# Performance work log

Hardware: AMD Instinct MI355X
Metric: run time of the kernel (lower is better)

## Reference

```python
import jax, jax.numpy as jnp
import numpy as np

D_MODEL = 256
D_STATE = 256
BATCH = 32
SEQ = 4096
RMIN, RMAX = 0.9, 0.999
NEG_SLOPE = 0.01
EPS = 1e-5


def layer_norm(x, w=None, b=None):
    m = jnp.mean(x, axis=-1, keepdims=True)
    v = jnp.var(x, axis=-1, keepdims=True)
    y = (x - m) * jax.lax.rsqrt(v + EPS)
    if w is not None:
        y = y * w + b
    return y


def leaky_relu(x):
    return jnp.where(x >= 0, x, NEG_SLOPE * x)


def setup_inputs() -> dict:
    key = jax.random.key(0)
    ks = jax.random.split(key, 12)
    x = jax.random.normal(ks[0], (BATCH, SEQ, D_MODEL), dtype=jnp.float32)
    # LRU ring init: |lambda| uniform in [rmin, rmax], phase uniform in [0, 2pi]
    u1 = jax.random.uniform(ks[1], (D_STATE,), dtype=jnp.float32)
    u2 = jax.random.uniform(ks[2], (D_STATE,), dtype=jnp.float32)
    nu_log = jnp.log(-0.5 * jnp.log(u1 * (RMAX**2 - RMIN**2) + RMIN**2))
    theta_log = jnp.log(2 * jnp.pi * u2)
    lam_mod = jnp.exp(-jnp.exp(nu_log))
    gamma_log = jnp.log(jnp.sqrt(1.0 - lam_mod**2))
    B_re = jax.random.normal(ks[3], (D_STATE, D_MODEL)) / np.sqrt(2 * D_MODEL)
    B_im = jax.random.normal(ks[4], (D_STATE, D_MODEL)) / np.sqrt(2 * D_MODEL)
    C_re = jax.random.normal(ks[5], (D_STATE, D_STATE)) / np.sqrt(D_STATE)
    C_im = jax.random.normal(ks[6], (D_STATE, D_STATE)) / np.sqrt(D_STATE)
    Dm = jax.random.normal(ks[7], (D_STATE, D_MODEL)) / np.sqrt(D_MODEL)
    Wl = jax.random.normal(ks[8], (D_MODEL, D_STATE)) / np.sqrt(D_STATE)
    bl = jax.random.normal(ks[9], (D_MODEL,)) * 0.02
    Wr = jax.random.normal(ks[10], (D_MODEL, D_STATE)) / np.sqrt(D_STATE)
    br = jax.random.normal(ks[11], (D_MODEL,)) * 0.02
    ones_m = jnp.ones((D_MODEL,), jnp.float32)
    zeros_m = jnp.zeros((D_MODEL,), jnp.float32)
    ones_s = jnp.ones((D_STATE,), jnp.float32)
    zeros_s = jnp.zeros((D_STATE,), jnp.float32)
    return {
        "x": x,
        "ln1_w": ones_m, "ln1_b": zeros_m,
        "nu_log": nu_log, "theta_log": theta_log, "gamma_log": gamma_log,
        "B_re": B_re, "B_im": B_im, "C_re": C_re, "C_im": C_im, "Dm": Dm,
        "ln2_w": ones_s, "ln2_b": zeros_s,
        "Wl": Wl, "bl": bl, "Wr": Wr, "br": br,
        "ln4_w": ones_m, "ln4_b": zeros_m,
    }


def reference(x, ln1_w, ln1_b, nu_log, theta_log, gamma_log, B_re, B_im,
              C_re, C_im, Dm, ln2_w, ln2_b, Wl, bl, Wr, br, ln4_w, ln4_b):
    # pre-norm + residual skip
    x1 = layer_norm(x, ln1_w, ln1_b)          # [B, T, d_model]
    skip = x1
    u = leaky_relu(x1)
    # LRU: h_t = lambda * h_{t-1} + gamma * (B u_t); y = Re(C h) + D u
    lam_mod = jnp.exp(-jnp.exp(nu_log))
    theta = jnp.exp(theta_log)
    lr = lam_mod * jnp.cos(theta)             # [N]
    li = lam_mod * jnp.sin(theta)
    gam = jnp.exp(gamma_log)
    bu_re = gam * jnp.einsum('btd,nd->btn', u, B_re)  # [B, T, N]
    bu_im = gam * jnp.einsum('btd,nd->btn', u, B_im)
    bu_re_t = jnp.swapaxes(bu_re, 0, 1)       # [T, B, N]
    bu_im_t = jnp.swapaxes(bu_im, 0, 1)

    def step(carry, inp):
        hr, hi = carry
        br_t, bi_t = inp
        hr2 = lr * hr - li * hi + br_t
        hi2 = lr * hi + li * hr + bi_t
        return (hr2, hi2), (hr2, hi2)

    h0 = (jnp.zeros((x.shape[0], lr.shape[0]), x.dtype),
          jnp.zeros((x.shape[0], lr.shape[0]), x.dtype))
    (hr_last, hi_last), (hr, hi) = jax.lax.scan(step, h0, (bu_re_t, bu_im_t))
    hr = jnp.swapaxes(hr, 0, 1)               # [B, T, N]
    hi = jnp.swapaxes(hi, 0, 1)
    y = (jnp.einsum('btn,mn->btm', hr, C_re)
         - jnp.einsum('btn,mn->btm', hi, C_im)
         + jnp.einsum('btd,md->btm', u, Dm))  # [B, T, d_state]
    # post-norm + nonlinearity
    y = leaky_relu(layer_norm(y, ln2_w, ln2_b))
    # gated bilinear MLP
    xl = layer_norm(y @ Wl.T + bl)            # no affine
    xr = layer_norm(y @ Wr.T + br)
    out = layer_norm(xl * xr, ln4_w, ln4_b) + skip
    return out
```

## Files before the change

### kernel.cpp

```cpp
#include <hip/hip_runtime.h>
#include <cstdint>
#include <cstddef>

#define DEV __device__ __forceinline__

typedef unsigned short u16;
typedef short short8 __attribute__((ext_vector_type(8)));
typedef float floatx4 __attribute__((ext_vector_type(4)));

constexpr int BB = 32;
constexpr int TT = 4096;
constexpr int RR = BB * TT;
constexpr int CH = 64;
constexpr int LC = TT / CH;

constexpr size_t OFF_LAM  = 0;
constexpr size_t OFF_LAML = 2048;
constexpr size_t OFF_GAM  = 4096;
constexpr size_t OFF_B1   = 8192;
constexpr size_t OFF_B2   = OFF_B1 + (size_t)512 * 256 * 2;
constexpr size_t OFF_B3   = OFF_B2 + (size_t)256 * 768 * 2;
constexpr size_t OFF_BIG  = 2ull << 20;
constexpr size_t SZB      = (size_t)RR * 256 * 2;

DEV float bf2f(u16 u) {
    unsigned int i = ((unsigned int)u) << 16;
    float f;
    __builtin_memcpy(&f, &i, 4);
    return f;
}
DEV u16 f2bf(float f) {
    unsigned int i;
    __builtin_memcpy(&i, &f, 4);
    i += 0x7fffu + ((i >> 16) & 1u);
    return (u16)(i >> 16);
}

DEV void gload16(const void* g, void* l) {
    __builtin_amdgcn_global_load_lds(
        (const __attribute__((address_space(1))) unsigned int*)g,
        (__attribute__((address_space(3))) unsigned int*)l, 16, 0, 0);
}

__global__ __launch_bounds__(256)
void k_setup(const float* __restrict__ nu_log, const float* __restrict__ theta_log,
             const float* __restrict__ gamma_log,
             const float* __restrict__ B_re, const float* __restrict__ B_im,
             const float* __restrict__ C_re, const float* __restrict__ C_im,
             const float* __restrict__ Dm,
             const float* __restrict__ Wl, const float* __restrict__ Wr,
             char* __restrict__ ws)
{
    float2* lam  = (float2*)(ws + OFF_LAM);
    float2* lamL = (float2*)(ws + OFF_LAML);
    float*  gam  = (float*)(ws + OFF_GAM);
    u16* B1 = (u16*)(ws + OFF_B1);
    u16* B2 = (u16*)(ws + OFF_B2);
    u16* B3 = (u16*)(ws + OFF_B3);
    int g = blockIdx.x * 256 + threadIdx.x;
    int stride = gridDim.x * 256;
    if (g < 256) {
        float mod = expf(-expf(nu_log[g]));
        float th  = expf(theta_log[g]);
        float lr = mod * cosf(th), li = mod * sinf(th);
        lam[g] = make_float2(lr, li);
        gam[g] = expf(gamma_log[g]);
        float pr = 1.f, pi = 0.f;
        for (int i = 0; i < LC; i++) { float nr = pr*lr - pi*li; pi = pr*li + pi*lr; pr = nr; }
        lamL[g] = make_float2(pr, pi);
    }
    for (int i = g; i < 512*256; i += stride) {
        int n = i >> 8, d = i & 255;
        B1[i] = f2bf(n < 256 ? B_re[n*256 + d] : B_im[(n-256)*256 + d]);
    }
    for (int i = g; i < 256*768; i += stride) {
        int m = i / 768, k = i - m*768;
        float v = (k < 256) ? C_re[m*256 + k]
                : (k < 512) ? -C_im[m*256 + (k-256)]
                            : Dm[m*256 + (k-512)];
        B2[i] = f2bf(v);
    }
    for (int i = g; i < 512*256; i += stride) {
        int n = i >> 8, d = i & 255;
        B3[i] = f2bf(n < 256 ? Wl[n*256 + d] : Wr[(n-256)*256 + d]);
    }
}

__global__ __launch_bounds__(256)
void k_ln1(const float* __restrict__ x, const float* __restrict__ w, const float* __restrict__ b,
           u16* __restrict__ u, u16* __restrict__ skip)
{
    const int wv = threadIdx.x >> 6, lane = threadIdx.x & 63;
    const size_t row = (size_t)blockIdx.x * 4 + wv;
    float4 v = ((const float4*)(x + row * 256))[lane];
    float s = v.x + v.y + v.z + v.w;
    float q = v.x*v.x + v.y*v.y + v.z*v.z + v.w*v.w;
    #pragma unroll
    for (int o = 32; o; o >>= 1) { s += __shfl_xor(s, o); q += __shfl_xor(q, o); }
    const float m  = s * (1.f/256.f);
    const float rs = rsqrtf(q * (1.f/256.f) - m*m + 1e-5f);
    const float4 wv4 = ((const float4*)w)[lane];
    const float4 bv4 = ((const float4*)b)[lane];
    float y0 = (v.x - m) * rs * wv4.x + bv4.x;
    float y1 = (v.y - m) * rs * wv4.y + bv4.y;
    float y2 = (v.z - m) * rs * wv4.z + bv4.z;
    float y3 = (v.w - m) * rs * wv4.w + bv4.w;
    ((ushort4*)(skip + row * 256))[lane] = make_ushort4(f2bf(y0), f2bf(y1), f2bf(y2), f2bf(y3));
    float u0 = y0 >= 0.f ? y0 : 0.01f * y0;
    float u1 = y1 >= 0.f ? y1 : 0.01f * y1;
    float u2 = y2 >= 0.f ? y2 : 0.01f * y2;
    float u3 = y3 >= 0.f ? y3 : 0.01f * y3;
    ((ushort4*)(u + row * 256))[lane] = make_ushort4(f2bf(u0), f2bf(u1), f2bf(u2), f2bf(u3));
}

__global__ __launch_bounds__(256)
void k_gemm1(const u16* __restrict__ A0, const u16* __restrict__ Bmat,
             u16* __restrict__ O0, u16* __restrict__ O1, const float* __restrict__ p0)
{
    __shared__ alignas(16) u16 As[2][128 * 64];
    __shared__ alignas(16) u16 Bs[2][128 * 64];
    const int wid = threadIdx.x >> 6, lane = threadIdx.x & 63;
    const int rowbase = blockIdx.x * 128;
    const int ct = blockIdx.y;
    const u16* Bbase = Bmat + (size_t)ct * 128 * 256;
    const int srow  = lane >> 3;
    const int sslot = (lane & 7) ^ srow;
    floatx4 acc[4][4] = {};

    auto stage = [&](int kt, int pb) {
        int kofs = kt * 64;
        #pragma unroll
        for (int i = 0; i < 4; i++) {
            int grp = wid * 4 + i;
            int row = grp * 8 + srow;
            gload16(A0 + (size_t)(rowbase + row) * 256 + kofs + sslot * 8,
                    (char*)&As[pb][0] + grp * 1024);
            gload16(Bbase + (size_t)row * 256 + kofs + sslot * 8,
                    (char*)&Bs[pb][0] + grp * 1024);
        }
    };

    stage(0, 0);
    const int wm = wid >> 1, wn = wid & 1;
    for (int kt = 0; kt < 4; ++kt) {
        const int pb = kt & 1;
        if (kt + 1 < 4) {
            stage(kt + 1, pb ^ 1);
            asm volatile("s_waitcnt vmcnt(8)" ::: "memory");
        } else {
            asm volatile("s_waitcnt vmcnt(0)" ::: "memory");
        }
        __builtin_amdgcn_s_barrier();
        short8 af[2][4], bfr[2][4];
        #pragma unroll
        for (int kk = 0; kk < 2; kk++) {
            const int rslot = (kk * 4 + (lane >> 4)) ^ (lane & 7);
            #pragma unroll
            for (int mi = 0; mi < 4; mi++)
                af[kk][mi] = *(const short8*)&As[pb][(wm*64 + mi*16 + (lane & 15)) * 64 + rslot * 8];
            #pragma unroll
            for (int ni = 0; ni < 4; ni++)
                bfr[kk][ni] = *(const short8*)&Bs[pb][(wn*64 + ni*16 + (lane & 15)) * 64 + rslot * 8];
        }
        #pragma unroll
        for (int mi = 0; mi < 4; mi++)
            #pragma unroll
            for (int ni = 0; ni < 4; ni++) {
                acc[mi][ni] = __builtin_amdgcn_mfma_f32_16x16x32_bf16(af[0][mi], bfr[0][ni], acc[mi][ni], 0, 0, 0);
                acc[mi][ni] = __builtin_amdgcn_mfma_f32_16x16x32_bf16(af[1][mi], bfr[1][ni], acc[mi][ni], 0, 0, 0);
            }
        __builtin_amdgcn_s_barrier();
    }
    #pragma unroll
    for (int mi = 0; mi < 4; mi++) {
        #pragma unroll
        for (int ni = 0; ni < 4; ni++) {
            const int cc = wn*64 + ni*16 + (lane & 15);
            const int n  = ct * 128 + cc;
            u16* outp = (n < 256) ? O0 : O1;
            const int col = n & 255;
            const float scale = p0[col];
            #pragma unroll
            for (int r = 0; r < 4; r++) {
                const int row = rowbase + wm*64 + mi*16 + ((lane >> 4) << 2) + r;
                outp[(size_t)row * 256 + col] = f2bf(acc[mi][ni][r] * scale);
            }
        }
    }
}

__global__ __launch_bounds__(512)
void k_gemm2(const u16* __restrict__ Ahr, const u16* __restrict__ Ahi, const u16* __restrict__ Au,
             const u16* __restrict__ Bm, u16* __restrict__ Oy,
             const float* __restrict__ w2, const float* __restrict__ b2)
{
    __shared__ alignas(16) char smem[49152 + 4096];
    u16*   As0 = (u16*)smem;
    u16*   Bs0 = (u16*)(smem + 16384);
    float* st  = (float*)(smem + 49152);
    const int tid = threadIdx.x, wid = tid >> 6, lane = tid & 63;
    const int lanelo = lane & 15, lanehi = lane >> 4;
    const int rowbase = blockIdx.x * 128;
    const int wm = wid >> 2, wn = wid & 3;
    floatx4 acc[4][4] = {};

    auto stage = [&](int kt, int pb) {
        const u16* Asrc = (kt < 8) ? Ahr : (kt < 16) ? Ahi : Au;
        const int kofs = (kt & 7) * 32;
        { int g = tid; int row = g >> 2, slot = g & 3;
          gload16(Asrc + (size_t)(rowbase + row) * 256 + kofs + slot * 8,
                  (char*)(As0 + pb * 4096) + (wid * 64) * 16); }
        #pragma unroll
        for (int j = 0; j < 2; j++) {
            int g = j * 512 + tid; int row = g >> 2, slot = g & 3;
            gload16(Bm + (size_t)row * 768 + kt * 32 + slot * 8,
                    (char*)(Bs0 + pb * 8192) + (j * 512 + wid * 64) * 16);
        }
    };

    stage(0, 0);
    for (int kt = 0; kt < 24; ++kt) {
        const int pb = kt & 1;
        if (kt + 1 < 24) {
            stage(kt + 1, pb ^ 1);
            asm volatile("s_waitcnt vmcnt(3)" ::: "memory");
        } else {
            asm volatile("s_waitcnt vmcnt(0)" ::: "memory");
        }
        __builtin_amdgcn_s_barrier();
        short8 af[4], bfr[4];
        #pragma unroll
        for (int mi = 0; mi < 4; mi++)
            af[mi] = *(const short8*)&As0[pb*4096 + (wm*64 + mi*16 + lanelo)*32 + lanehi*8];
        #pragma unroll
        for (int ni = 0; ni < 4; ni++)
            bfr[ni] = *(const short8*)&Bs0[pb*8192 + (wn*64 + ni*16 + lanelo)*32 + lanehi*8];
        #pragma unroll
        for (int mi = 0; mi < 4; mi++)
            #pragma unroll
            for (int ni = 0; ni < 4; ni++)
                acc[mi][ni] = __builtin_amdgcn_mfma_f32_16x16x32_bf16(af[mi], bfr[ni], acc[mi][ni], 0, 0, 0);
        __builtin_amdgcn_s_barrier();
    }

    float sarr[4][4], qarr[4][4];
    #pragma unroll
    for (int mi = 0; mi < 4; mi++)
        #pragma unroll
        for (int r = 0; r < 4; r++) {
            float s = 0.f, q = 0.f;
            #pragma unroll
            for (int ni = 0; ni < 4; ni++) { float v = acc[mi][ni][r]; s += v; q += v*v; }
            sarr[mi][r] = s; qarr[mi][r] = q;
        }
    #pragma unroll
    for (int o = 1; o < 16; o <<= 1)
        #pragma unroll
        for (int mi = 0; mi < 4; mi++)
            #pragma unroll
            for (int r = 0; r < 4; r++) {
                sarr[mi][r] += __shfl_xor(sarr[mi][r], o);
                qarr[mi][r] += __shfl_xor(qarr[mi][r], o);
            }
    if (lanelo == 0) {
        #pragma unroll
        for (int mi = 0; mi < 4; mi++)
            #pragma unroll
            for (int r = 0; r < 4; r++) {
                int rw = mi*16 + lanehi*4 + r;
                st[(wid*64 + rw)*2 + 0] = sarr[mi][r];
                st[(wid*64 + rw)*2 + 1] = qarr[mi][r];
            }
    }
    __syncthreads();
    float wc[4], bc[4];
    #pragma unroll
    for (int ni = 0; ni < 4; ni++) {
        int col = wn*64 + ni*16 + lanelo;
        wc[ni] = w2[col]; bc[ni] = b2[col];
    }
    #pragma unroll
    for (int mi = 0; mi < 4; mi++)
        #pragma unroll
        for (int r = 0; r < 4; r++) {
            const int rw = mi*16 + lanehi*4 + r;
            float S = 0.f, Q = 0.f;
            #pragma unroll
            for (int ww = 0; ww < 4; ww++) {
                S += st[((wm*4 + ww)*64 + rw)*2 + 0];
                Q += st[((wm*4 + ww)*64 + rw)*2 + 1];
            }
            const float m  = S * (1.f/256.f);
            const float rs = rsqrtf(Q * (1.f/256.f) - m*m + 1e-5f);
            const size_t row = (size_t)rowbase + wm*64 + rw;
            #pragma unroll
            for (int ni = 0; ni < 4; ni++) {
                int col = wn*64 + ni*16 + lanelo;
                float v = (acc[mi][ni][r] - m) * rs * wc[ni] + bc[ni];
                v = v >= 0.f ? v : 0.01f * v;
                Oy[row * 256 + col] = f2bf(v);
            }
        }
}

__global__ __launch_bounds__(1024)
void k_gemm3f(const u16* __restrict__ Ay, const u16* __restrict__ Bm,
              const float* __restrict__ bl, const float* __restrict__ brr,
              const float* __restrict__ w4, const float* __restrict__ b4,
              const u16* __restrict__ skip, float* __restrict__ out)
{
    __shared__ alignas(16) char smem[81920];
    u16*   As0 = (u16*)smem;
    u16*   Bs0 = (u16*)(smem + 16384);
    float* st  = (float*)smem;
    float* st4 = (float*)(smem + 16384);
    const int tid = threadIdx.x, wid = tid >> 6, lane = tid & 63;
    const int lanelo = lane & 15, lanehi = lane >> 4;
    const int rowbase = blockIdx.x * 128;
    const int wm = wid >> 3, wn = wid & 7;
    floatx4 acc[4][4] = {};

    auto stage = [&](int kt, int pb) {
        const int kofs = kt * 32;
        if (tid < 512) {
            int row = tid >> 2, slot = tid & 3;
            gload16(Ay + (size_t)(rowbase + row) * 256 + kofs + slot * 8,
                    (char*)(As0 + pb * 4096) + wid * 1024);
        }
        #pragma unroll
        for (int j = 0; j < 2; j++) {
            int g = j * 1024 + tid; int row = g >> 2, slot = g & 3;
            gload16(Bm + (size_t)row * 256 + kofs + slot * 8,
                    (char*)(Bs0 + pb * 16384) + (j * 1024 + wid * 64) * 16);
        }
    };

    stage(0, 0);
    for (int kt = 0; kt < 8; ++kt) {
        const int pb = kt & 1;
        if (kt + 1 < 8) {
            stage(kt + 1, pb ^ 1);
            if (wid < 8) asm volatile("s_waitcnt vmcnt(3)" ::: "memory");
            else         asm volatile("s_waitcnt vmcnt(2)" ::: "memory");
        } else {
            asm volatile("s_waitcnt vmcnt(0)" ::: "memory");
        }
        __builtin_amdgcn_s_barrier();
        short8 af[4], bfr[4];
        #pragma unroll
        for (int mi = 0; mi < 4; mi++)
            af[mi] = *(const short8*)&As0[pb*4096 + (wm*64 + mi*16 + lanelo)*32 + lanehi*8];
        #pragma unroll
        for (int ni = 0; ni < 4; ni++) {
            const int s = wn*32 + (ni&1)*16 + (ni>>1)*256 + lanelo;
            bfr[ni] = *(const short8*)&Bs0[pb*16384 + s*32 + lanehi*8];
        }
        #pragma unroll
        for (int mi = 0; mi < 4; mi++)
            #pragma unroll
            for (int ni = 0; ni < 4; ni++)
                acc[mi][ni] = __builtin_amdgcn_mfma_f32_16x16x32_bf16(af[mi], bfr[ni], acc[mi][ni], 0, 0, 0);
        __builtin_amdgcn_s_barrier();
    }
    __syncthreads();

    float bcl[2], bcr[2];
    #pragma unroll
    for (int j = 0; j < 2; j++) {
        const int cl = wn*32 + j*16 + lanelo;
        bcl[j] = bl[cl]; bcr[j] = brr[cl];
    }
    #pragma unroll
    for (int mi = 0; mi < 4; mi++)
        #pragma unroll
        for (int r = 0; r < 4; r++) {
            acc[mi][0][r] += bcl[0]; acc[mi][1][r] += bcl[1];
            acc[mi][2][r] += bcr[0]; acc[mi][3][r] += bcr[1];
        }
    #pragma unroll
    for (int mi = 0; mi < 4; mi++)
        #pragma unroll
        for (int r = 0; r < 4; r++) {
            float a0 = acc[mi][0][r], a1 = acc[mi][1][r];
            float b0 = acc[mi][2][r], b1 = acc[mi][3][r];
            float sLv = a0 + a1, qLv = a0*a0 + a1*a1;
            float sRv = b0 + b1, qRv = b0*b0 + b1*b1;
            #pragma unroll
            for (int o = 1; o < 16; o <<= 1) {
                sLv += __shfl_xor(sLv, o); qLv += __shfl_xor(qLv, o);
                sRv += __shfl_xor(sRv, o); qRv += __shfl_xor(qRv, o);
            }
            if (lanelo == 0) {
                const int rw = mi*16 + lanehi*4 + r;
                float* p = &st[(wid*64 + rw)*4];
                p[0] = sLv; p[1] = qLv; p[2] = sRv; p[3] = qRv;
            }
        }
    __syncthreads();
    #pragma unroll
    for (int mi = 0; mi < 4; mi++)
        #pragma unroll
        for (int r = 0; r < 4; r++) {
            const int rw = mi*16 + lanehi*4 + r;
            float SL = 0.f, QL = 0.f, SR = 0.f, QR = 0.f;
            #pragma unroll
            for (int ww = 0; ww < 8; ww++) {
                const float* p = &st[((wm*8 + ww)*64 + rw)*4];
                SL += p[0]; QL += p[1]; SR += p[2]; QR += p[3];
            }
            const float mL = SL * (1.f/256.f);
            const float rsL = rsqrtf(QL * (1.f/256.f) - mL*mL + 1e-5f);
            const float mR = SR * (1.f/256.f);
            const float rsR = rsqrtf(QR * (1.f/256.f) - mR*mR + 1e-5f);
            float p0 = ((acc[mi][0][r] - mL) * rsL) * ((acc[mi][2][r] - mR) * rsR);
            float p1 = ((acc[mi][1][r] - mL) * rsL) * ((acc[mi][3][r] - mR) * rsR);
            acc[mi][0][r] = p0; acc[mi][1][r] = p1;
            float s4 = p0 + p1, q4 = p0*p0 + p1*p1;
            #pragma unroll
            for (int o = 1; o < 16; o <<= 1) {
                s4 += __shfl_xor(s4, o); q4 += __shfl_xor(q4, o);
            }
            if (lanelo == 0) {
                float* p = &st4[(wid*64 + rw)*2];
                p[0] = s4; p[1] = q4;
            }
        }
    __syncthreads();
    float w4c[2], b4c[2];
    #pragma unroll
    for (int j = 0; j < 2; j++) {
        const int col = wn*32 + j*16 + lanelo;
        w4c[j] = w4[col]; b4c[j] = b4[col];
    }
    #pragma unroll
    for (int mi = 0; mi < 4; mi++)
        #pragma unroll
        for (int r = 0; r < 4; r++) {
            const int rw = mi*16 + lanehi*4 + r;
            float S4 = 0.f, Q4 = 0.f;
            #pragma unroll
            for (int ww = 0; ww < 8; ww++) {
                const float* p = &st4[((wm*8 + ww)*64 + rw)*2];
                S4 += p[0]; Q4 += p[1];
            }
            const float m4 = S4 * (1.f/256.f);
            const float rs4 = rsqrtf(Q4 * (1.f/256.f) - m4*m4 + 1e-5f);
            const size_t row = (size_t)rowbase + wm*64 + rw;
            #pragma unroll
            for (int j = 0; j < 2; j++) {
                const int col = wn*32 + j*16 + lanelo;
                float o = (acc[mi][j][r] - m4) * rs4 * w4c[j] + b4c[j]
                        + bf2f(skip[row*256 + col]);
                out[row*256 + col] = o;
            }
        }
}

__global__ __launch_bounds__(128)
void k_scan1(const u16* __restrict__ bre, const u16* __restrict__ bim,
             float4* __restrict__ carry, const char* __restrict__ ws)
{
    const float2* lam = (const float2*)(ws + OFF_LAM);
    const int b = blockIdx.x, c = blockIdx.y, p = threadIdx.x;
    const unsigned int* pre = (const unsigned int*)bre;
    const unsigned int* pim = (const unsigned int*)bim;
    const float2 l0 = lam[2*p], l1 = lam[2*p + 1];
    float hr0 = 0, hi0 = 0, hr1 = 0, hi1 = 0;
    size_t base = ((size_t)b * TT + (size_t)c * LC) * 128 + p;
    #pragma unroll 8
    for (int j = 0; j < LC; j++) {
        unsigned int re = pre[base + (size_t)j * 128];
        unsigned int im = pim[base + (size_t)j * 128];
        float br0 = bf2f((u16)(re & 0xffff)), br1 = bf2f((u16)(re >> 16));
        float bi0 = bf2f((u16)(im & 0xffff)), bi1 = bf2f((u16)(im >> 16));
        float nr0 = fmaf(l0.x, hr0, fmaf(-l0.y, hi0, br0));
        float ni0 = fmaf(l0.x, hi0, fmaf( l0.y, hr0, bi0));
        float nr1 = fmaf(l1.x, hr1, fmaf(-l1.y, hi1, br1));
        float ni1 = fmaf(l1.x, hi1, fmaf( l1.y, hr1, bi1));
        hr0 = nr0; hi0 = ni0; hr1 = nr1; hi1 = ni1;
    }
    carry[((size_t)b * CH + c) * 128 + p] = make_float4(hr0, hi0, hr1, hi1);
}

__global__ __launch_bounds__(128)
void k_comb(float4* __restrict__ carry, const char* __restrict__ ws)
{
    const float2* lamL = (const float2*)(ws + OFF_LAML);
    const int b = blockIdx.x, p = threadIdx.x;
    const float2 L0 = lamL[2*p], L1 = lamL[2*p + 1];
    float4 prev = make_float4(0.f, 0.f, 0.f, 0.f);
    size_t base = (size_t)b * CH * 128 + p;
    float4 nxt = carry[base];
    for (int c = 0; c < CH; c++) {
        float4 cur = nxt;
        if (c + 1 < CH) nxt = carry[base + (size_t)(c + 1) * 128];
        carry[base + (size_t)c * 128] = prev;
        float nx = fmaf(L0.x, prev.x, fmaf(-L0.y, prev.y, cur.x));
        float ny = fmaf(L0.x, prev.y, fmaf( L0.y, prev.x, cur.y));
        float nz = fmaf(L1.x, prev.z, fmaf(-L1.y, prev.w, cur.z));
        float nw = fmaf(L1.x, prev.w, fmaf( L1.y, prev.z, cur.w));
        prev = make_float4(nx, ny, nz, nw);
    }
}

__global__ __launch_bounds__(128)
void k_scan2(u16* __restrict__ bre, u16* __restrict__ bim,
             const float4* __restrict__ carry, const char* __restrict__ ws)
{
    const float2* lam = (const float2*)(ws + OFF_LAM);
    const int b = blockIdx.x, c = blockIdx.y, p = threadIdx.x;
    unsigned int* pre = (unsigned int*)bre;
    unsigned int* pim = (unsigned int*)bim;
    const float2 l0 = lam[2*p], l1 = lam[2*p + 1];
    float4 h0 = carry[((size_t)b * CH + c) * 128 + p];
    float hr0 = h0.x, hi0 = h0.y, hr1 = h0.z, hi1 = h0.w;
    size_t base = ((size_t)b * TT + (size_t)c * LC) * 128 + p;
    #pragma unroll 8
    for (int j = 0; j < LC; j++) {
        size_t idx = base + (size_t)j * 128;
        unsigned int re = pre[idx];
        unsigned int im = pim[idx];
        float br0 = bf2f((u16)(re & 0xffff)), br1 = bf2f((u16)(re >> 16));
        float bi0 = bf2f((u16)(im & 0xffff)), bi1 = bf2f((u16)(im >> 16));
        float nr0 = fmaf(l0.x, hr0, fmaf(-l0.y, hi0, br0));
        float ni0 = fmaf(l0.x, hi0, fmaf( l0.y, hr0, bi0));
        float nr1 = fmaf(l1.x, hr1, fmaf(-l1.y, hi1, br1));
        float ni1 = fmaf(l1.x, hi1, fmaf( l1.y, hr1, bi1));
        hr0 = nr0; hi0 = ni0; hr1 = nr1; hi1 = ni1;
        pre[idx] = ((unsigned int)f2bf(hr1) << 16) | f2bf(hr0);
        pim[idx] = ((unsigned int)f2bf(hi1) << 16) | f2bf(hi0);
    }
}

extern "C" void kernel_launch(void* const* d_in, const int* in_sizes, int n_in,
                              void* d_out, int out_size, void* d_ws, size_t ws_size,
                              hipStream_t stream)
{
    (void)in_sizes; (void)n_in; (void)out_size; (void)ws_size;
    const float* x         = (const float*)d_in[0];
    const float* ln1_w     = (const float*)d_in[1];
    const float* ln1_b     = (const float*)d_in[2];
    const float* nu_log    = (const float*)d_in[3];
    const float* theta_log = (const float*)d_in[4];
    const float* gamma_log = (const float*)d_in[5];
    const float* B_re      = (const float*)d_in[6];
    const float* B_im      = (const float*)d_in[7];
    const float* C_re      = (const float*)d_in[8];
    const float* C_im      = (const float*)d_in[9];
    const float* Dm        = (const float*)d_in[10];
    const float* ln2_w     = (const float*)d_in[11];
    const float* ln2_b     = (const float*)d_in[12];
    const float* Wl        = (const float*)d_in[13];
    const float* bl        = (const float*)d_in[14];
    const float* Wr        = (const float*)d_in[15];
    const float* br        = (const float*)d_in[16];
    const float* ln4_w     = (const float*)d_in[17];
    const float* ln4_b     = (const float*)d_in[18];

    char* ws = (char*)d_ws;
    float* gam = (float*)(ws + OFF_GAM);
    u16* B1 = (u16*)(ws + OFF_B1);
    u16* B2 = (u16*)(ws + OFF_B2);
    u16* B3 = (u16*)(ws + OFF_B3);
    u16* u    = (u16*)(ws + OFF_BIG);
    u16* skip = (u16*)(ws + OFF_BIG + 1 * SZB);
    u16* bure = (u16*)(ws + OFF_BIG + 2 * SZB);
    u16* buim = (u16*)(ws + OFF_BIG + 3 * SZB);
    u16* y    = (u16*)(ws + OFF_BIG + 4 * SZB);
    float4* carry = (float4*)(ws + OFF_BIG + 5 * SZB);
    float* out = (float*)d_out;

    k_setup<<<dim3(256), dim3(256), 0, stream>>>(nu_log, theta_log, gamma_log,
                                                 B_re, B_im, C_re, C_im, Dm, Wl, Wr, ws);
    k_ln1<<<dim3(RR/4), dim3(256), 0, stream>>>(x, ln1_w, ln1_b, u, skip);
    k_gemm1<<<dim3(RR/128, 4), dim3(256), 0, stream>>>(u, B1, bure, buim, gam);
    k_scan1<<<dim3(BB, CH), dim3(128), 0, stream>>>(bure, buim, carry, ws);
    k_comb<<<dim3(BB), dim3(128), 0, stream>>>(carry, ws);
    k_scan2<<<dim3(BB, CH), dim3(128), 0, stream>>>(bure, buim, carry, ws);
    k_gemm2<<<dim3(RR/128), dim3(512), 0, stream>>>(bure, buim, u, B2, y, ln2_w, ln2_b);
    k_gemm3f<<<dim3(RR/128), dim3(1024), 0, stream>>>(y, B3, bl, br, ln4_w, ln4_b, skip, out);
}
```

Measured before the change: 479.6 us.

## Split fused gated-MLP GEMM into tiled GEMM plus separate layernorm epilogue kernel

Replaces the single 1024-thread fused GEMM+triple-layernorm kernel with a 256-thread swizzled, double-buffered GEMM that writes bf16 xl/xr (bias added) into the reused bure/buim buffers. A new row-wise kernel then does the two layernorms, the product, the final layernorm and the skip add. This trades extra global traffic (writing and rereading two bf16 intermediates) for a leaner GEMM with better occupancy and no cross-wave LDS reductions. It also rounds the pre-norm activations to bf16.

```diff
diff --git a/kernel.cpp b/kernel.cpp
--- a/kernel.cpp
+++ b/kernel.cpp
@@ -189,6 +189,83 @@
     }
 }
 
+__global__ __launch_bounds__(256)
+void k_gemm3(const u16* __restrict__ A0, const u16* __restrict__ Bmat,
+             u16* __restrict__ O0, u16* __restrict__ O1,
+             const float* __restrict__ p0, const float* __restrict__ p1)
+{
+    __shared__ alignas(16) u16 As[2][128 * 64];
+    __shared__ alignas(16) u16 Bs[2][128 * 64];
+    const int wid = threadIdx.x >> 6, lane = threadIdx.x & 63;
+    const int rowbase = blockIdx.x * 128;
+    const int ct = blockIdx.y;
+    const u16* Bbase = Bmat + (size_t)ct * 128 * 256;
+    const int srow  = lane >> 3;
+    const int sslot = (lane & 7) ^ srow;
+    floatx4 acc[4][4] = {};
+
+    auto stage = [&](int kt, int pb) {
+        int kofs = kt * 64;
+        #pragma unroll
+        for (int i = 0; i < 4; i++) {
+            int grp = wid * 4 + i;
+            int row = grp * 8 + srow;
+            gload16(A0 + (size_t)(rowbase + row) * 256 + kofs + sslot * 8,
+                    (char*)&As[pb][0] + grp * 1024);
+            gload16(Bbase + (size_t)row * 256 + kofs + sslot * 8,
+                    (char*)&Bs[pb][0] + grp * 1024);
+        }
+    };
+
+    stage(0, 0);
+    const int wm = wid >> 1, wn = wid & 1;
+    for (int kt = 0; kt < 4; ++kt) {
+        const int pb = kt & 1;
+        if (kt + 1 < 4) {
+            stage(kt + 1, pb ^ 1);
+            asm volatile("s_waitcnt vmcnt(8)" ::: "memory");
+        } else {
+            asm volatile("s_waitcnt vmcnt(0)" ::: "memory");
+        }
+        __builtin_amdgcn_s_barrier();
+        short8 af[2][4], bfr[2][4];
+        #pragma unroll
+        for (int kk = 0; kk < 2; kk++) {
+            const int rslot = (kk * 4 + (lane >> 4)) ^ (lane & 7);
+            #pragma unroll
+            for (int mi = 0; mi < 4; mi++)
+                af[kk][mi] = *(const short8*)&As[pb][(wm*64 + mi*16 + (lane & 15)) * 64 + rslot * 8];
+            #pragma unroll
+            for (int ni = 0; ni < 4; ni++)
+                bfr[kk][ni] = *(const short8*)&Bs[pb][(wn*64 + ni*16 + (lane & 15)) * 64 + rslot * 8];
+        }
+        #pragma unroll
+        for (int mi = 0; mi < 4; mi++)
+            #pragma unroll
+            for (int ni = 0; ni < 4; ni++) {
+                acc[mi][ni] = __builtin_amdgcn_mfma_f32_16x16x32_bf16(af[0][mi], bfr[0][ni], acc[mi][ni], 0, 0, 0);
+                acc[mi][ni] = __builtin_amdgcn_mfma_f32_16x16x32_bf16(af[1][mi], bfr[1][ni], acc[mi][ni], 0, 0, 0);
+            }
+        __builtin_amdgcn_s_barrier();
+    }
+    #pragma unroll
+    for (int mi = 0; mi < 4; mi++) {
+        #pragma unroll
+        for (int ni = 0; ni < 4; ni++) {
+            const int cc = wn*64 + ni*16 + (lane & 15);
+            const int n  = ct * 128 + cc;
+            u16* outp = (n < 256) ? O0 : O1;
+            const int col = n & 255;
+            const float badd = (n < 256 ? p0 : p1)[col];
+            #pragma unroll
+            for (int r = 0; r < 4; r++) {
+                const int row = rowbase + wm*64 + mi*16 + ((lane >> 4) << 2) + r;
+                outp[(size_t)row * 256 + col] = f2bf(acc[mi][ni][r] + badd);
+            }
+        }
+    }
+}
+
 __global__ __launch_bounds__(512)
 void k_gemm2(const u16* __restrict__ Ahr, const u16* __restrict__ Ahi, const u16* __restrict__ Au,
              const u16* __restrict__ Bm, u16* __restrict__ Oy,
@@ -303,157 +380,41 @@
         }
 }
 
-__global__ __launch_bounds__(1024)
-void k_gemm3f(const u16* __restrict__ Ay, const u16* __restrict__ Bm,
-              const float* __restrict__ bl, const float* __restrict__ brr,
-              const float* __restrict__ w4, const float* __restrict__ b4,
-              const u16* __restrict__ skip, float* __restrict__ out)
-{
-    __shared__ alignas(16) char smem[81920];
-    u16*   As0 = (u16*)smem;
-    u16*   Bs0 = (u16*)(smem + 16384);
-    float* st  = (float*)smem;
-    float* st4 = (float*)(smem + 16384);
-    const int tid = threadIdx.x, wid = tid >> 6, lane = tid & 63;
-    const int lanelo = lane & 15, lanehi = lane >> 4;
-    const int rowbase = blockIdx.x * 128;
-    const int wm = wid >> 3, wn = wid & 7;
-    floatx4 acc[4][4] = {};
-
-    auto stage = [&](int kt, int pb) {
-        const int kofs = kt * 32;
-        if (tid < 512) {
-            int row = tid >> 2, slot = tid & 3;
-            gload16(Ay + (size_t)(rowbase + row) * 256 + kofs + slot * 8,
-                    (char*)(As0 + pb * 4096) + wid * 1024);
-        }
-        #pragma unroll
-        for (int j = 0; j < 2; j++) {
-            int g = j * 1024 + tid; int row = g >> 2, slot = g & 3;
-            gload16(Bm + (size_t)row * 256 + kofs + slot * 8,
-                    (char*)(Bs0 + pb * 16384) + (j * 1024 + wid * 64) * 16);
-        }
-    };
-
-    stage(0, 0);
-    for (int kt = 0; kt < 8; ++kt) {
-        const int pb = kt & 1;
-        if (kt + 1 < 8) {
-            stage(kt + 1, pb ^ 1);
-            if (wid < 8) asm volatile("s_waitcnt vmcnt(3)" ::: "memory");
-            else         asm volatile("s_waitcnt vmcnt(2)" ::: "memory");
-        } else {
-            asm volatile("s_waitcnt vmcnt(0)" ::: "memory");
-        }
-        __builtin_amdgcn_s_barrier();
-        short8 af[4], bfr[4];
-        #pragma unroll
-        for (int mi = 0; mi < 4; mi++)
-            af[mi] = *(const short8*)&As0[pb*4096 + (wm*64 + mi*16 + lanelo)*32 + lanehi*8];
-        #pragma unroll
-        for (int ni = 0; ni < 4; ni++) {
-            const int s = wn*32 + (ni&1)*16 + (ni>>1)*256 + lanelo;
-            bfr[ni] = *(const short8*)&Bs0[pb*16384 + s*32 + lanehi*8];
-        }
-        #pragma unroll
-        for (int mi = 0; mi < 4; mi++)
-            #pragma unroll
-            for (int ni = 0; ni < 4; ni++)
-                acc[mi][ni] = __builtin_amdgcn_mfma_f32_16x16x32_bf16(af[mi], bfr[ni], acc[mi][ni], 0, 0, 0);
-        __builtin_amdgcn_s_barrier();
-    }
-    __syncthreads();
-
-    float bcl[2], bcr[2];
-    #pragma unroll
-    for (int j = 0; j < 2; j++) {
-        const int cl = wn*32 + j*16 + lanelo;
-        bcl[j] = bl[cl]; bcr[j] = brr[cl];
-    }
-    #pragma unroll
-    for (int mi = 0; mi < 4; mi++)
-        #pragma unroll
-        for (int r = 0; r < 4; r++) {
-            acc[mi][0][r] += bcl[0]; acc[mi][1][r] += bcl[1];
-            acc[mi][2][r] += bcr[0]; acc[mi][3][r] += bcr[1];
-        }
-    #pragma unroll
-    for (int mi = 0; mi < 4; mi++)
-        #pragma unroll
-        for (int r = 0; r < 4; r++) {
-            float a0 = acc[mi][0][r], a1 = acc[mi][1][r];
-            float b0 = acc[mi][2][r], b1 = acc[mi][3][r];
-            float sLv = a0 + a1, qLv = a0*a0 + a1*a1;
-            float sRv = b0 + b1, qRv = b0*b0 + b1*b1;
-            #pragma unroll
-            for (int o = 1; o < 16; o <<= 1) {
-                sLv += __shfl_xor(sLv, o); qLv += __shfl_xor(qLv, o);
-                sRv += __shfl_xor(sRv, o); qRv += __shfl_xor(qRv, o);
-            }
-            if (lanelo == 0) {
-                const int rw = mi*16 + lanehi*4 + r;
-                float* p = &st[(wid*64 + rw)*4];
-                p[0] = sLv; p[1] = qLv; p[2] = sRv; p[3] = qRv;
-            }
-        }
-    __syncthreads();
-    #pragma unroll
-    for (int mi = 0; mi < 4; mi++)
-        #pragma unroll
-        for (int r = 0; r < 4; r++) {
-            const int rw = mi*16 + lanehi*4 + r;
-            float SL = 0.f, QL = 0.f, SR = 0.f, QR = 0.f;
-            #pragma unroll
-            for (int ww = 0; ww < 8; ww++) {
-                const float* p = &st[((wm*8 + ww)*64 + rw)*4];
-                SL += p[0]; QL += p[1]; SR += p[2]; QR += p[3];
-            }
-            const float mL = SL * (1.f/256.f);
-            const float rsL = rsqrtf(QL * (1.f/256.f) - mL*mL + 1e-5f);
-            const float mR = SR * (1.f/256.f);
-            const float rsR = rsqrtf(QR * (1.f/256.f) - mR*mR + 1e-5f);
-            float p0 = ((acc[mi][0][r] - mL) * rsL) * ((acc[mi][2][r] - mR) * rsR);
-            float p1 = ((acc[mi][1][r] - mL) * rsL) * ((acc[mi][3][r] - mR) * rsR);
-            acc[mi][0][r] = p0; acc[mi][1][r] = p1;
-            float s4 = p0 + p1, q4 = p0*p0 + p1*p1;
-            #pragma unroll
-            for (int o = 1; o < 16; o <<= 1) {
-                s4 += __shfl_xor(s4, o); q4 += __shfl_xor(q4, o);
-            }
-            if (lanelo == 0) {
-                float* p = &st4[(wid*64 + rw)*2];
-                p[0] = s4; p[1] = q4;
-            }
-        }
-    __syncthreads();
-    float w4c[2], b4c[2];
-    #pragma unroll
-    for (int j = 0; j < 2; j++) {
-        const int col = wn*32 + j*16 + lanelo;
-        w4c[j] = w4[col]; b4c[j] = b4[col];
-    }
-    #pragma unroll
-    for (int mi = 0; mi < 4; mi++)
-        #pragma unroll
-        for (int r = 0; r < 4; r++) {
-            const int rw = mi*16 + lanehi*4 + r;
-            float S4 = 0.f, Q4 = 0.f;
-            #pragma unroll
-            for (int ww = 0; ww < 8; ww++) {
-                const float* p = &st4[((wm*8 + ww)*64 + rw)*2];
-                S4 += p[0]; Q4 += p[1];
-            }
-            const float m4 = S4 * (1.f/256.f);
-            const float rs4 = rsqrtf(Q4 * (1.f/256.f) - m4*m4 + 1e-5f);
-            const size_t row = (size_t)rowbase + wm*64 + rw;
-            #pragma unroll
-            for (int j = 0; j < 2; j++) {
-                const int col = wn*32 + j*16 + lanelo;
-                float o = (acc[mi][j][r] - m4) * rs4 * w4c[j] + b4c[j]
-                        + bf2f(skip[row*256 + col]);
-                out[row*256 + col] = o;
-            }
-        }
+__global__ __launch_bounds__(256)
+void k_final(const u16* __restrict__ gl, const u16* __restrict__ gr, const u16* __restrict__ skip,
+             const float* __restrict__ w4, const float* __restrict__ b4, float* __restrict__ out)
+{
+    const int wv = threadIdx.x >> 6, lane = threadIdx.x & 63;
+    const size_t row = (size_t)blockIdx.x * 4 + wv;
+    ushort4 ra = ((const ushort4*)(gl + row * 256))[lane];
+    ushort4 rc = ((const ushort4*)(gr + row * 256))[lane];
+    float a0 = bf2f(ra.x), a1 = bf2f(ra.y), a2 = bf2f(ra.z), a3 = bf2f(ra.w);
+    float c0 = bf2f(rc.x), c1 = bf2f(rc.y), c2 = bf2f(rc.z), c3 = bf2f(rc.w);
+    float s1 = a0+a1+a2+a3, q1 = a0*a0+a1*a1+a2*a2+a3*a3;
+    float s2 = c0+c1+c2+c3, q2 = c0*c0+c1*c1+c2*c2+c3*c3;
+    #pragma unroll
+    for (int o = 32; o; o >>= 1) {
+        s1 += __shfl_xor(s1, o); q1 += __shfl_xor(q1, o);
+        s2 += __shfl_xor(s2, o); q2 += __shfl_xor(q2, o);
+    }
+    const float m1 = s1*(1.f/256.f), rs1 = rsqrtf(q1*(1.f/256.f) - m1*m1 + 1e-5f);
+    const float m2 = s2*(1.f/256.f), rs2 = rsqrtf(q2*(1.f/256.f) - m2*m2 + 1e-5f);
+    float v0 = ((a0-m1)*rs1) * ((c0-m2)*rs2);
+    float v1 = ((a1-m1)*rs1) * ((c1-m2)*rs2);
+    float v2 = ((a2-m1)*rs1) * ((c2-m2)*rs2);
+    float v3 = ((a3-m1)*rs1) * ((c3-m2)*rs2);
+    float s3 = v0+v1+v2+v3, q3 = v0*v0+v1*v1+v2*v2+v3*v3;
+    #pragma unroll
+    for (int o = 32; o; o >>= 1) { s3 += __shfl_xor(s3, o); q3 += __shfl_xor(q3, o); }
+    const float m3 = s3*(1.f/256.f), rs3 = rsqrtf(q3*(1.f/256.f) - m3*m3 + 1e-5f);
+    const float4 wv4 = ((const float4*)w4)[lane];
+    const float4 bv4 = ((const float4*)b4)[lane];
+    ushort4 sk = ((const ushort4*)(skip + row * 256))[lane];
+    float o0 = (v0-m3)*rs3*wv4.x + bv4.x + bf2f(sk.x);
+    float o1 = (v1-m3)*rs3*wv4.y + bv4.y + bf2f(sk.y);
+    float o2 = (v2-m3)*rs3*wv4.z + bv4.z + bf2f(sk.z);
+    float o3 = (v3-m3)*rs3*wv4.w + bv4.w + bf2f(sk.w);
+    ((float4*)(out + row * 256))[lane] = make_float4(o0, o1, o2, o3);
 }
 
 __global__ __launch_bounds__(128)
@@ -578,5 +539,6 @@
     k_comb<<<dim3(BB), dim3(128), 0, stream>>>(carry, ws);
     k_scan2<<<dim3(BB, CH), dim3(128), 0, stream>>>(bure, buim, carry, ws);
     k_gemm2<<<dim3(RR/128), dim3(512), 0, stream>>>(bure, buim, u, B2, y, ln2_w, ln2_b);
-    k_gemm3f<<<dim3(RR/128), dim3(1024), 0, stream>>>(y, B3, bl, br, ln4_w, ln4_b, skip, out);
-}
+    k_gemm3<<<dim3(RR/128, 4), dim3(256), 0, stream>>>(y, B3, bure, buim, bl, br);
+    k_final<<<dim3(RR/4), dim3(256), 0, stream>>>(bure, buim, skip, ln4_w, ln4_b, out);
+}
```

Result: faster. 427.6 us (-10.8%).
